# Performance work log

Measured on AMD Instinct MI355X. Metric: run time of the kernel, lower is better.

Reference implementation:

```python
import jax, jax.numpy as jnp
import numpy as np

N_NODES = 10000
N_EDGES = 160000
B = 128
HEADS = 4
DIMS = [36, 128, 256, 512]
NEG_SLOPE = 0.2  # PyG GATConv default


def setup_inputs() -> dict:
    key = jax.random.key(0)
    ks = jax.random.split(key, 32)
    inp = {}
    inp["x"] = jax.random.normal(ks[0], (N_NODES, DIMS[0]), jnp.float32)
    inp["edge_index"] = jax.random.randint(ks[1], (2, N_EDGES), 0, N_NODES)
    inp["batch"] = jnp.sort(jax.random.randint(ks[2], (N_NODES,), 0, B))
    ki = 3
    for i in range(3):
        din, dout = DIMS[i], DIMS[i + 1]
        C = dout // HEADS
        inp[f"gcn_w{i}"] = jax.random.normal(ks[ki], (din, dout), jnp.float32) * (din ** -0.5); ki += 1
        inp[f"gcn_b{i}"] = jnp.zeros((dout,), jnp.float32)
        inp[f"gat_w{i}"] = jax.random.normal(ks[ki], (dout, dout), jnp.float32) * (dout ** -0.5); ki += 1
        inp[f"gat_as{i}"] = jax.random.normal(ks[ki], (HEADS, C), jnp.float32) * 0.1; ki += 1
        inp[f"gat_ad{i}"] = jax.random.normal(ks[ki], (HEADS, C), jnp.float32) * 0.1; ki += 1
        inp[f"gat_b{i}"] = jnp.zeros((dout,), jnp.float32)
    D = DIMS[-1]
    inp["ap_w1"] = jax.random.normal(ks[ki], (D, D // 2), jnp.float32) * (D ** -0.5); ki += 1
    inp["ap_b1"] = jnp.zeros((D // 2,), jnp.float32)
    inp["ap_w2"] = jax.random.normal(ks[ki], (D // 2, 1), jnp.float32) * ((D // 2) ** -0.5); ki += 1
    inp["ap_b2"] = jnp.zeros((1,), jnp.float32)
    return inp


def _gcn(x, w, b, src, dst, n):
    # PyG GCNConv: add self-loops, symmetric deg^-1/2 normalization, bias after agg
    h = x @ w  # [N, dout]
    deg = jax.ops.segment_sum(jnp.ones_like(dst, dtype=h.dtype), dst, n) + 1.0  # incl. self-loop
    dinv = deg ** -0.5
    norm = dinv[src] * dinv[dst]  # [E]
    agg = jax.ops.segment_sum(h[src] * norm[:, None], dst, n)
    agg = agg + h * (dinv * dinv)[:, None]  # self-loop messages
    return agg + b


def _gat(x, w, a_s, a_d, b, src, dst, n):
    # PyG GATConv: self-loops, leaky-relu logits, segment softmax over dst, concat heads
    C = w.shape[1] // HEADS
    h = (x @ w).reshape(n, HEADS, C)
    alpha_src = (h * a_s).sum(-1)  # [N, H]
    alpha_dst = (h * a_d).sum(-1)  # [N, H]
    loop = jnp.arange(n)
    s = jnp.concatenate([src, loop])
    d = jnp.concatenate([dst, loop])
    e = jax.nn.leaky_relu(alpha_src[s] + alpha_dst[d], NEG_SLOPE)  # [E+N, H]
    m = jax.ops.segment_max(e, d, n)
    ex = jnp.exp(e - m[d])
    den = jax.ops.segment_sum(ex, d, n)
    alpha = ex / den[d]  # [E+N, H]
    out = jax.ops.segment_sum(h[s] * alpha[:, :, None], d, n)  # [N, H, C]
    return out.reshape(n, HEADS * C) + b


def _forward(x, edge_index, batch, params, ap_w1, ap_b1, ap_w2, ap_b2):
    src, dst = edge_index[0], edge_index[1]
    n = x.shape[0]
    x_in = x
    n_layers = len(params)
    for i, (gw, gb, aw, a_s, a_d, ab) in enumerate(params):
        h = jax.nn.relu(_gcn(x, gw, gb, src, dst, n))  # dropout is identity in eval
        x = h + _gat(h, aw, a_s, a_d, ab, src, dst, n)
        if i < n_layers - 1:
            if x.shape[-1] == x_in.shape[-1]:
                x = x + x_in
            x_in = x
    # attention pooling (global softmax then per-graph masked renorm)
    a = jnp.tanh(x @ ap_w1 + ap_b1) @ ap_w2 + ap_b2  # [N, 1]
    a = jax.nn.softmax(a, axis=0)
    mask = jax.nn.one_hot(batch, B, dtype=x.dtype)  # [N, B]
    aw_ = a * mask
    aw_ = aw_ / (aw_.sum(0, keepdims=True) + 1e-8)
    graph_emb = aw_.T @ x  # [B, D]
    cnt = jax.ops.segment_sum(jnp.ones((n,), x.dtype), batch, B)
    ssum = jax.ops.segment_sum(x, batch, B)
    mean = ssum / jnp.maximum(cnt, 1.0)[:, None]
    smax = jax.ops.segment_max(x, batch, B)
    return jnp.concatenate([graph_emb, mean, smax, ssum], axis=1)  # [B, 4*D]


def reference(x, edge_index, batch,
              gcn_w0, gcn_b0, gat_w0, gat_as0, gat_ad0, gat_b0,
              gcn_w1, gcn_b1, gat_w1, gat_as1, gat_ad1, gat_b1,
              gcn_w2, gcn_b2, gat_w2, gat_as2, gat_ad2, gat_b2,
              ap_w1, ap_b1, ap_w2, ap_b2):
    params = [
        (gcn_w0, gcn_b0, gat_w0, gat_as0, gat_ad0, gat_b0),
        (gcn_w1, gcn_b1, gat_w1, gat_as1, gat_ad1, gat_b1),
        (gcn_w2, gcn_b2, gat_w2, gat_as2, gat_ad2, gat_b2),
    ]
    return _forward(x, edge_index, batch, params, ap_w1, ap_b1, ap_w2, ap_b2)
```

## Files before the change

### kernel.cpp

```cpp
#include <hip/hip_runtime.h>
#include <math.h>

#define NN 10000
#define NE 160000
#define NB 128
#define NH 4
#define DOUT 512
#define NEG 0.2f
#define CNT_BLKS ((NE + 255) / 256)

typedef __attribute__((ext_vector_type(8))) short short8;
typedef __attribute__((ext_vector_type(4))) float f32x4;
typedef __attribute__((ext_vector_type(4))) unsigned short us4;

__device__ __forceinline__ float leakyf(float v){ return fmaxf(v, NEG*v); }
__device__ __forceinline__ void fma4(float4& a, const float4 v, float w){
  a.x += v.x*w; a.y += v.y*w; a.z += v.z*w; a.w += v.w*w;
}
__device__ __forceinline__ unsigned short f2bf(float f){
  unsigned int u = __float_as_uint(f);
  u += 0x7FFFu + ((u >> 16) & 1u);
  return (unsigned short)(u >> 16);
}
__device__ __forceinline__ float bf2f(unsigned short h){
// ... 7 lines not shown
                                         size_t base, float4 v){
  us4 h, l; unsigned short hh, ll;
  split2(v.x, hh, ll); h[0]=hh; l[0]=ll;
  split2(v.y, hh, ll); h[1]=hh; l[1]=ll;
  split2(v.z, hh, ll); h[2]=hh; l[2]=ll;
  split2(v.w, hh, ll); h[3]=hh; l[3]=ll;
  *(us4*)&H[base] = h;
  *(us4*)&L[base] = l;
}
__device__ __forceinline__ void gl_lds16(const unsigned short* g, unsigned short* l){
  __builtin_amdgcn_global_load_lds(
      (const __attribute__((address_space(1))) unsigned int*)g,
      (__attribute__((address_space(3))) unsigned int*)l, 16, 0, 0);
}

struct AllConv {
  const float* src[7];
  unsigned short* dh[7];
  unsigned short* dl[7];
  int K[7], Mm[7], Kp[7], tot[7];
};

__global__ void k_count_conv(const int* __restrict__ dst, int* __restrict__ cnt,
                             AllConv a, int convTot){
  int bid = blockIdx.x;
  if (bid < CNT_BLKS){
    int e = bid*256 + threadIdx.x;
    if (e < NE) atomicAdd(&cnt[dst[e]], 1);
  } else {
    int idx = (bid - CNT_BLKS)*256 + threadIdx.x;
    if (idx >= convTot) return;
    int j = 0;
    while (idx >= a.tot[j]){ idx -= a.tot[j]; j++; }
    int Kp = a.Kp[j], K = a.K[j], M = a.Mm[j];
    int kk = idx % Kp, m = idx / Kp;
    float v = (kk < K) ? a.src[j][(size_t)kk*M + m] : 0.f;
    unsigned short h, l; split2(v, h, l);
    a.dh[j][idx] = h; a.dl[j][idx] = l;
  }
}

__global__ __launch_bounds__(1024) void k_scan_all(
    const int* __restrict__ cnt, const int* __restrict__ batch,
    int* __restrict__ rowptr, float* __restrict__ dinv,
    int* __restrict__ cursor, float* __restrict__ apre,
    int* __restrict__ starts){
  __shared__ int sh[NN];
  __shared__ int pref[1024];
  int t = threadIdx.x;
  for (int i = t; i < NN; i += 1024) sh[i] = cnt[i];
  if (t <= NB){
    int lo = 0, hi = NN;
    while (lo < hi){ int mid = (lo + hi) >> 1; if (batch[mid] < t) lo = mid + 1; else hi = mid; }
    starts[t] = lo;
  }
  __syncthreads();
  int base = t*10;
  int csum = 0;
#pragma unroll
  for (int k = 0; k < 10; k++){ int i = base + k; if (i < NN) csum += sh[i]; }
  pref[t] = csum; __syncthreads();
  for (int o = 1; o < 1024; o <<= 1){
    int v = (t >= o) ? pref[t - o] : 0;
    __syncthreads();
    pref[t] += v;
    __syncthreads();
  }
  int run = pref[t] - csum;
#pragma unroll
  for (int k = 0; k < 10; k++){
    int i = base + k;
    if (i < NN){
      int c = sh[i];
      rowptr[i] = run;
      run += c;
      dinv[i] = rsqrtf((float)c + 1.f);
      cursor[i] = 0;
      apre[i] = 0.f;
    }
  }
  if (t == 1023) rowptr[NN] = pref[1023];
}

__global__ void k_fill(const int* __restrict__ src, const int* __restrict__ dst,
                       const int* __restrict__ rowptr, int* __restrict__ cursor,
                       int* __restrict__ colidx){
  int e = blockIdx.x*blockDim.x + threadIdx.x;
  if (e >= NE) return;
  int d = dst[e];
  int pos = atomicAdd(&cursor[d], 1);
  colidx[rowptr[d] + pos] = src[e];
}

#define GBM 64
#define GBN 128
#define GBK 64
__global__ __launch_bounds__(256) void k_gemm_bf3(
    const unsigned short* __restrict__ Ah, const unsigned short* __restrict__ Al,
    const unsigned short* __restrict__ Bh, const unsigned short* __restrict__ Bl,
    float* __restrict__ C, int N, int Kp, int M, int mode,
    const float* __restrict__ bias, unsigned short* __restrict__ outH,
    unsigned short* __restrict__ outL,
    const float* __restrict__ a_s, const float* __restrict__ a_d,
    float* __restrict__ as_o, float* __restrict__ ad_o, int Cdim){
  __shared__ unsigned short AsH[2*GBM*32], AsL[2*GBM*32];
  __shared__ unsigned short BsH[2*GBN*32], BsL[2*GBN*32];
  __shared__ float sred[2][GBM][4];
  int gx = M / GBN;
  int gy = (N + GBM - 1) / GBM;
  const int G = 8;
  int bid = blockIdx.x;
  int full = gy / G;
  int bid_full = full * G * gx;
  int by, bx;
  if (bid < bid_full){
    int g = bid / (G*gx); int rem = bid % (G*gx);
    by = g*G + rem % G; bx = rem / G;
  } else {
    int rem = bid - bid_full; int rows = gy - full*G;
    by = full*G + rem % rows; bx = rem / rows;
  }
  int row0 = by * GBM, col0 = bx * GBN;
  int t = threadIdx.x;
  int w = t >> 6, L = t & 63;
  int lm = L & 15, lq = L >> 4;
  int wc = w * 32;
// ... 24 lines not shown
  int nk = Kp / GBK;
  for (int kt = 0; kt < nk; kt++){
    int k0 = kt * GBK;
    if (kt) __syncthreads();
#pragma unroll
    for (int h = 0; h < 2; h++){
      int kh = k0 + h*32;
      gl_lds16(&Ah[(size_t)agrow*Kp + kh + ga*8],  &AsH[h*2048 + w*512]);
      gl_lds16(&Al[(size_t)agrow*Kp + kh + ga*8],  &AsL[h*2048 + w*512]);
      gl_lds16(&Bh[(size_t)bgrow0*Kp + kh + gb0*8], &BsH[h*4096 + w*512]);
      gl_lds16(&Bh[(size_t)bgrow1*Kp + kh + gb1*8], &BsH[h*4096 + (w+4)*512]);
      gl_lds16(&Bl[(size_t)bgrow0*Kp + kh + gb0*8], &BsL[h*4096 + w*512]);
      gl_lds16(&Bl[(size_t)bgrow1*Kp + kh + gb1*8], &BsL[h*4096 + (w+4)*512]);
    }
    __syncthreads();

#pragma unroll
    for (int h = 0; h < 2; h++){
      short8 ah[4], al[4], bh[2], bl[2];
#pragma unroll
      for (int mi = 0; mi < 4; mi++){
        ah[mi] = *(const short8*)&AsH[h*2048 + aoff[mi]];
        al[mi] = *(const short8*)&AsL[h*2048 + aoff[mi]];
      }
#pragma unroll
      for (int ni = 0; ni < 2; ni++){
        bh[ni] = *(const short8*)&BsH[h*4096 + boff[ni]];
        bl[ni] = *(const short8*)&BsL[h*4096 + boff[ni]];
      }
#pragma unroll
      for (int mi = 0; mi < 4; mi++)
// ... 40 lines not shown
    float sA0 = a_s[col0 + wc + lm], sA1 = a_s[col0 + wc + 16 + lm];
    float dA0 = a_d[col0 + wc + lm], dA1 = a_d[col0 + wc + 16 + lm];
#pragma unroll
    for (int mi = 0; mi < 4; mi++)
#pragma unroll
      for (int r = 0; r < 4; r++){
        float vs = acc[mi][0][r]*sA0 + acc[mi][1][r]*sA1;
        float vd = acc[mi][0][r]*dA0 + acc[mi][1][r]*dA1;
#pragma unroll
        for (int o = 1; o <= 8; o <<= 1){
          vs += __shfl_xor(vs, o);
          vd += __shfl_xor(vd, o);
        }
        if (lm == 0){
          int row = mi*16 + lq*4 + r;
          sred[0][row][w] = vs;
          sred[1][row][w] = vd;
        }
      }
    __syncthreads();
    if (t < GBM){
      int n = row0 + t;
      if (n < N){
        int wph = Cdim >> 5;
        int nheads = 4 / wph;
        for (int g = 0; g < nheads; g++){
          float ss = 0.f, dd = 0.f;
          for (int q = 0; q < wph; q++){
            ss += sred[0][t][g*wph + q];
            dd += sred[1][t][g*wph + q];
          }
          int hd = (col0 + g*wph*32) / Cdim;
          as_o[n*NH + hd] = ss;
          ad_o[n*NH + hd] = dd;
        }
      }
    }
  } else if (mode == 3){
    float b0 = bias[col0 + wc + lm], b1v = bias[col0 + wc + 16 + lm];
    float w0v = a_s[col0 + wc + lm], w1v = a_s[col0 + wc + 16 + lm];
#pragma unroll
    for (int mi = 0; mi < 4; mi++)
#pragma unroll
      for (int r = 0; r < 4; r++){
        float v = tanhf(acc[mi][0][r] + b0)*w0v + tanhf(acc[mi][1][r] + b1v)*w1v;
#pragma unroll
        for (int o = 1; o <= 8; o <<= 1) v += __shfl_xor(v, o);
        if (lm == 0) sred[0][mi*16 + lq*4 + r][w] = v;
      }
    __syncthreads();
    if (t < GBM){
      int n = row0 + t;
      if (n < N){
        float s = sred[0][t][0] + sred[0][t][1] + sred[0][t][2] + sred[0][t][3];
        atomicAdd(&as_o[n], s);
      }
    }
  }
}

__global__ __launch_bounds__(256) void k_gcn_pre0(
    const float* __restrict__ x0, const float* __restrict__ dinv,
    const int* __restrict__ rowptr, const int* __restrict__ colidx,
    unsigned short* __restrict__ outH, unsigned short* __restrict__ outL){
  int t = threadIdx.x;
  int sub = t & 15;
  int n = blockIdx.x*16 + (t >> 4);
  if (n >= NN) return;
  int f0 = sub*4;
  bool act = f0 < 36;
  int b = rowptr[n], e = rowptr[n+1];
  float dn = dinv[n];
  float4 a0 = make_float4(0,0,0,0), a1 = make_float4(0,0,0,0);
  float4 a2 = make_float4(0,0,0,0), a3 = make_float4(0,0,0,0);
  if (act){
    float4 sv = *(const float4*)&x0[(size_t)n*36 + f0];
    int j = b;
    for (; j + 7 < e; j += 8){
      int s0 = colidx[j],   s1 = colidx[j+1], s2 = colidx[j+2], s3 = colidx[j+3];
      int s4 = colidx[j+4], s5 = colidx[j+5], s6 = colidx[j+6], s7 = colidx[j+7];
      float w0 = dinv[s0], w1 = dinv[s1], w2 = dinv[s2], w3 = dinv[s3];
      float w4 = dinv[s4], w5 = dinv[s5], w6 = dinv[s6], w7 = dinv[s7];
      float4 v0 = *(const float4*)&x0[(size_t)s0*36 + f0];
      float4 v1 = *(const float4*)&x0[(size_t)s1*36 + f0];
      float4 v2 = *(const float4*)&x0[(size_t)s2*36 + f0];
      float4 v3 = *(const float4*)&x0[(size_t)s3*36 + f0];
      float4 v4 = *(const float4*)&x0[(size_t)s4*36 + f0];
// ... 12 lines not shown
      float4 v1 = *(const float4*)&x0[(size_t)s1*36 + f0];
      float4 v2 = *(const float4*)&x0[(size_t)s2*36 + f0];
      float4 v3 = *(const float4*)&x0[(size_t)s3*36 + f0];
      fma4(a0, v0, w0*dn); fma4(a1, v1, w1*dn);
      fma4(a2, v2, w2*dn); fma4(a3, v3, w3*dn);
    }
    for (; j < e; j++){
      int s = colidx[j];
      float4 v = *(const float4*)&x0[(size_t)s*36 + f0];
      fma4(a0, v, dinv[s]*dn);
    }
    float4 acc = make_float4(a0.x+a1.x+a2.x+a3.x, a0.y+a1.y+a2.y+a3.y,
                             a0.z+a1.z+a2.z+a3.z, a0.w+a1.w+a2.w+a3.w);
    float dn2 = dn*dn;
    acc.x += sv.x*dn2; acc.y += sv.y*dn2; acc.z += sv.z*dn2; acc.w += sv.w*dn2;
    store_hl(outH, outL, (size_t)n*64 + f0, acc);
  } else {
    store_hl(outH, outL, (size_t)n*64 + f0, make_float4(0,0,0,0));
  }
}

__global__ __launch_bounds__(256) void k_gcn_pre(
    const float* __restrict__ xf, const float* __restrict__ dinv,
    const int* __restrict__ rowptr, const int* __restrict__ colidx,
    unsigned short* __restrict__ outH, unsigned short* __restrict__ outL,
    int Kp, int nchunk){
  int bid = blockIdx.x;
  int chunk = bid % nchunk, grp = bid / nchunk;
  int t = threadIdx.x;
  int sub = t & 15;
  int n = grp*16 + (t >> 4);
  if (n >= NN) return;
  int f0 = chunk*64 + sub*4;
  int b = rowptr[n], e = rowptr[n+1];
  float dn = dinv[n];
  float4 sv = *(const float4*)&xf[(size_t)n*Kp + f0];
  float4 a0 = make_float4(0,0,0,0), a1 = make_float4(0,0,0,0);
  float4 a2 = make_float4(0,0,0,0), a3 = make_float4(0,0,0,0);
  int j = b;
  for (; j + 7 < e; j += 8){
    int s0 = colidx[j],   s1 = colidx[j+1], s2 = colidx[j+2], s3 = colidx[j+3];
    int s4 = colidx[j+4], s5 = colidx[j+5], s6 = colidx[j+6], s7 = colidx[j+7];
    float w0 = dinv[s0], w1 = dinv[s1], w2 = dinv[s2], w3 = dinv[s3];
    float w4 = dinv[s4], w5 = dinv[s5], w6 = dinv[s6], w7 = dinv[s7];
    float4 v0 = *(const float4*)&xf[(size_t)s0*Kp + f0];
    float4 v1 = *(const float4*)&xf[(size_t)s1*Kp + f0];
    float4 v2 = *(const float4*)&xf[(size_t)s2*Kp + f0];
    float4 v3 = *(const float4*)&xf[(size_t)s3*Kp + f0];
    float4 v4 = *(const float4*)&xf[(size_t)s4*Kp + f0];
    float4 v5 = *(const float4*)&xf[(size_t)s5*Kp + f0];
// ... 11 lines not shown
    float4 v1 = *(const float4*)&xf[(size_t)s1*Kp + f0];
    float4 v2 = *(const float4*)&xf[(size_t)s2*Kp + f0];
    float4 v3 = *(const float4*)&xf[(size_t)s3*Kp + f0];
    fma4(a0, v0, w0*dn); fma4(a1, v1, w1*dn);
    fma4(a2, v2, w2*dn); fma4(a3, v3, w3*dn);
  }
  for (; j < e; j++){
    int s = colidx[j];
    float4 v = *(const float4*)&xf[(size_t)s*Kp + f0];
    fma4(a0, v, dinv[s]*dn);
  }
  float4 acc = make_float4(a0.x+a1.x+a2.x+a3.x, a0.y+a1.y+a2.y+a3.y,
                           a0.z+a1.z+a2.z+a3.z, a0.w+a1.w+a2.w+a3.w);
  float dn2 = dn*dn;
  acc.x += sv.x*dn2; acc.y += sv.y*dn2; acc.z += sv.z*dn2; acc.w += sv.w*dn2;
  store_hl(outH, outL, (size_t)n*Kp + f0, acc);
}

__global__ __launch_bounds__(256) void k_gat_gather(
    const float* __restrict__ hg, const float* __restrict__ hf,
    const int* __restrict__ rowptr, const int* __restrict__ colidx,
    const float* __restrict__ as_, const float* __restrict__ ad_,
    const float* __restrict__ ab,
    unsigned short* __restrict__ outH, unsigned short* __restrict__ outL,
    float* __restrict__ xf,
    int M, int C, int nchunk){
  int bid = blockIdx.x;
  int chunk = bid % nchunk, grp = bid / nchunk;
  int t = threadIdx.x;
  int sub = t & 15;
  int n = grp*16 + (t >> 4);
  if (n >= NN) return;
  int f0 = chunk*64 + sub*4;
  int hd = f0 / C;
  int b = rowptr[n], e = rowptr[n+1];
  int ai = n*NH + hd;
  float adn = ad_[ai];
  float sl = fminf(fmaxf(leakyf(as_[ai] + adn), -80.f), 80.f);
  float es = __expf(sl);
  float4 sv = *(const float4*)&hg[(size_t)n*M + f0];
  float4 hv = *(const float4*)&hf[(size_t)n*M + f0];
  float4 bb = *(const float4*)&ab[f0];
  float d = es;
  float4 a0 = make_float4(0,0,0,0), a1 = make_float4(0,0,0,0);
  float4 a2 = make_float4(0,0,0,0), a3 = make_float4(0,0,0,0);
  int j = b;
  for (; j + 7 < e; j += 8){
    int s0 = colidx[j],   s1 = colidx[j+1], s2 = colidx[j+2], s3 = colidx[j+3];
    int s4 = colidx[j+4], s5 = colidx[j+5], s6 = colidx[j+6], s7 = colidx[j+7];
    float l0 = leakyf(as_[s0*NH + hd] + adn), l1 = leakyf(as_[s1*NH + hd] + adn);
    float l2 = leakyf(as_[s2*NH + hd] + adn), l3 = leakyf(as_[s3*NH + hd] + adn);
    float l4 = leakyf(as_[s4*NH + hd] + adn), l5 = leakyf(as_[s5*NH + hd] + adn);
    float l6 = leakyf(as_[s6*NH + hd] + adn), l7 = leakyf(as_[s7*NH + hd] + adn);
    float4 v0 = *(const float4*)&hg[(size_t)s0*M + f0];
    float4 v1 = *(const float4*)&hg[(size_t)s1*M + f0];
    float4 v2 = *(const float4*)&hg[(size_t)s2*M + f0];
    float4 v3 = *(const float4*)&hg[(size_t)s3*M + f0];
// ... 15 lines not shown
    int s = colidx[j];
    float l = leakyf(as_[s*NH + hd] + adn);
    float4 v = *(const float4*)&hg[(size_t)s*M + f0];
    float ww = __expf(fminf(fmaxf(l,-80.f),80.f));
    d += ww;
    fma4(a0, v, ww);
  }
  float4 acc = make_float4(a0.x+a1.x+a2.x+a3.x, a0.y+a1.y+a2.y+a3.y,
                           a0.z+a1.z+a2.z+a3.z, a0.w+a1.w+a2.w+a3.w);
  float inv = 1.f/d;
  float4 r = make_float4(
    hv.x + bb.x + (sv.x*es + acc.x)*inv,
    hv.y + bb.y + (sv.y*es + acc.y)*inv,
    hv.z + bb.z + (sv.z*es + acc.z)*inv,
    hv.w + bb.w + (sv.w*es + acc.w)*inv);
  *(float4*)&xf[(size_t)n*M + f0] = r;
  store_hl(outH, outL, (size_t)n*M + f0, r);
}

__global__ __launch_bounds__(512) void k_pool(
    const float* __restrict__ xf,
    const float* __restrict__ apre, const int* __restrict__ starts,
    float* __restrict__ out){
  __shared__ float red[512];
  __shared__ float4 comb[3][4][128];
  int g = blockIdx.x, t = threadIdx.x;
  int b = starts[g], e = starts[g+1];
  float m = -INFINITY;
  for (int n = b + t; n < e; n += 512) m = fmaxf(m, apre[n]);
  red[t] = m; __syncthreads();
  for (int o = 256; o > 0; o >>= 1){
    if (t < o) red[t] = fmaxf(red[t], red[t + o]);
    __syncthreads();
  }
  m = red[0]; __syncthreads();
  float s = 0.f;
  for (int n = b + t; n < e; n += 512) s += __expf(apre[n] - m);
  red[t] = s; __syncthreads();
  for (int o = 256; o > 0; o >>= 1){
    if (t < o) red[t] += red[t + o];
    __syncthreads();
  }
  float inv = 1.f / (red[0] + 1e-8f);
  int lf = t & 127, sl = t >> 7;
  float4 sum = make_float4(0,0,0,0), wacc = make_float4(0,0,0,0);
  float4 mx = make_float4(-INFINITY,-INFINITY,-INFINITY,-INFINITY);
  for (int n = b + sl; n < e; n += 4){
    float4 xv = *(const float4*)&xf[(size_t)n*DOUT + lf*4];
    float p = __expf(apre[n] - m) * inv;
    sum.x += xv.x; sum.y += xv.y; sum.z += xv.z; sum.w += xv.w;
    mx.x = fmaxf(mx.x, xv.x); mx.y = fmaxf(mx.y, xv.y);
    mx.z = fmaxf(mx.z, xv.z); mx.w = fmaxf(mx.w, xv.w);
    fma4(wacc, xv, p);
  }
  comb[0][sl][lf] = wacc; comb[1][sl][lf] = sum; comb[2][sl][lf] = mx;
  __syncthreads();
  if (sl == 0){
#pragma unroll
    for (int q = 1; q < 4; q++){
      float4 w2 = comb[0][q][lf], s2 = comb[1][q][lf], m2 = comb[2][q][lf];
      wacc.x += w2.x; wacc.y += w2.y; wacc.z += w2.z; wacc.w += w2.w;
      sum.x += s2.x; sum.y += s2.y; sum.z += s2.z; sum.w += s2.w;
      mx.x = fmaxf(mx.x, m2.x); mx.y = fmaxf(mx.y, m2.y);
      mx.z = fmaxf(mx.z, m2.z); mx.w = fmaxf(mx.w, m2.w);
    }
    float ic = 1.f / fmaxf((float)(e - b), 1.f);
    float4* o = (float4*)(out + (size_t)g*4*DOUT);
    o[lf]       = wacc;
    o[128 + lf] = make_float4(sum.x*ic, sum.y*ic, sum.z*ic, sum.w*ic);
    o[256 + lf] = mx;
    o[384 + lf] = sum;
  }
}

extern "C" void kernel_launch(void* const* d_in, const int* in_sizes, int n_in,
                              void* d_out, int out_size, void* d_ws, size_t ws_size,
                              hipStream_t stream) {
  const float* x0   = (const float*)d_in[0];
  const int*   ei   = (const int*)d_in[1];
  const int*   src  = ei;
  const int*   dst  = ei + NE;
  const int*   batch= (const int*)d_in[2];
  const float* gw[3]  = {(const float*)d_in[3],  (const float*)d_in[9],  (const float*)d_in[15]};
  const float* gb[3]  = {(const float*)d_in[4],  (const float*)d_in[10], (const float*)d_in[16]};
  const float* aw[3]  = {(const float*)d_in[5],  (const float*)d_in[11], (const float*)d_in[17]};
  const float* asw[3] = {(const float*)d_in[6],  (const float*)d_in[12], (const float*)d_in[18]};
  const float* adw[3] = {(const float*)d_in[7],  (const float*)d_in[13], (const float*)d_in[19]};
  const float* ab[3]  = {(const float*)d_in[8],  (const float*)d_in[14], (const float*)d_in[20]};
  const float* apw1 = (const float*)d_in[21];
  const float* apb1 = (const float*)d_in[22];
  const float* apw2 = (const float*)d_in[23];
  float* out = (float*)d_out;

  char* p = (char*)d_ws;
  auto alloc = [&](size_t bytes) -> void* {
    void* r = (void*)p; p += (bytes + 255) & ~(size_t)255; return r;
  };
  float* f1 = (float*)alloc((size_t)NN*512*4);
  float* hf = (float*)alloc((size_t)NN*512*4);
  float* xf = (float*)alloc((size_t)NN*512*4);
  unsigned short* actH0 = (unsigned short*)alloc((size_t)NN*512*2);
  unsigned short* actL0 = (unsigned short*)alloc((size_t)NN*512*2);
  unsigned short* actH1 = (unsigned short*)alloc((size_t)NN*512*2);
  unsigned short* actL1 = (unsigned short*)alloc((size_t)NN*512*2);
  unsigned short* preH  = (unsigned short*)alloc((size_t)NN*256*2);
  unsigned short* preL  = (unsigned short*)alloc((size_t)NN*256*2);
  const int wK[7]  = {36, 128, 128, 256, 256, 512, 512};
  const int wM[7]  = {128, 128, 256, 256, 512, 512, 256};
  const int wKp[7] = {64, 128, 128, 256, 256, 512, 512};
  const float* wsrc[7] = {gw[0], aw[0], gw[1], aw[1], gw[2], aw[2], apw1};
  unsigned short* wTh[7]; unsigned short* wTl[7];
  for (int i = 0; i < 7; i++){
    size_t sz = (size_t)wM[i]*wKp[i]*2;
    wTh[i] = (unsigned short*)alloc(sz);
    wTl[i] = (unsigned short*)alloc(sz);
  }
  float* dinv = (float*)alloc(NN*4);
  float* as_  = (float*)alloc(NN*NH*4);
  float* ad_  = (float*)alloc(NN*NH*4);
  float* apre = (float*)alloc(NN*4);
  int* rowptr = (int*)alloc((NN+1)*4);
  int* colidx = (int*)alloc((size_t)NE*4);
  int* cnt    = (int*)alloc(NN*4);
  int* cursor = (int*)alloc(NN*4);
  int* starts = (int*)alloc((NB+1)*4);

  AllConv ac;
  int convTot = 0;
  for (int i = 0; i < 7; i++){
    ac.src[i] = wsrc[i]; ac.dh[i] = wTh[i]; ac.dl[i] = wTl[i];
    ac.K[i] = wK[i]; ac.Mm[i] = wM[i]; ac.Kp[i] = wKp[i];
    ac.tot[i] = wKp[i]*wM[i];
    convTot += ac.tot[i];
  }

  hipMemsetAsync(cnt, 0, NN*sizeof(int), stream);
  int convBlks = (convTot + 255) / 256;
  k_count_conv<<<CNT_BLKS + convBlks, 256, 0, stream>>>(dst, cnt, ac, convTot);
  k_scan_all<<<1, 1024, 0, stream>>>(cnt, batch, rowptr, dinv, cursor, apre, starts);
  k_fill<<<(NE+255)/256, 256, 0, stream>>>(src, dst, rowptr, cursor, colidx);

  const int dims[4] = {36, 128, 256, 512};
  const int ngrp = (NN + 15) / 16;
  int wi = 0;
  for (int i = 0; i < 3; i++){
    int Kin = (i == 0) ? 64 : dims[i];
    int M = dims[i+1], C = M/NH;
    int nchunk_in = Kin / 64;
    int nchunk = M / 64;
    int nblk = (M/GBN) * ((NN+GBM-1)/GBM);
    if (i == 0){
      k_gcn_pre0<<<ngrp, 256, 0, stream>>>(x0, dinv, rowptr, colidx, preH, preL);
    } else {
      k_gcn_pre<<<nchunk_in*ngrp, 256, 0, stream>>>(xf, dinv, rowptr, colidx,
                                                    preH, preL, Kin, nchunk_in);
    }
    k_gemm_bf3<<<nblk, 256, 0, stream>>>(preH, preL, wTh[wi], wTl[wi], hf, NN, wKp[wi], M,
                                         1, gb[i], actH0, actL0,
                                         nullptr, nullptr, nullptr, nullptr, C);
    wi++;
    k_gemm_bf3<<<nblk, 256, 0, stream>>>(actH0, actL0, wTh[wi], wTl[wi], f1, NN, wKp[wi], M,
                                         2, nullptr, nullptr, nullptr,
                                         asw[i], adw[i], as_, ad_, C);
    wi++;
    k_gat_gather<<<nchunk*ngrp, 256, 0, stream>>>(f1, hf, rowptr, colidx,
                                                  as_, ad_, ab[i],
                                                  actH1, actL1, xf, M, C, nchunk);
  }

  {
    int nblk = (256/GBN) * ((NN+GBM-1)/GBM);
    k_gemm_bf3<<<nblk, 256, 0, stream>>>(actH1, actL1, wTh[6], wTl[6], nullptr, NN, wKp[6], 256,
                                         3, apb1, nullptr, nullptr,
                                         apw2, nullptr, apre, nullptr, 64);
  }
  k_pool<<<NB, 512, 0, stream>>>(xf, apre, starts, out);
}
```

Baseline: 382.1 us.

## Fuse whole GNN pipeline into one cooperative persistent kernel with degree-sorted node order

Replaces the sequence of about 15 kernel launches with a single cooperative persistent kernel. Stages are separated by grid-wide syncs, and each stage distributes its GEMM, gather and pool tiles over the resident blocks. It adds a degree histogram in the scan that builds a permutation ordering nodes by descending degree, so gather tiles handle nodes of similar degree together and load imbalance drops. It also skips writing bf16 split activations for the first two GAT layers, where they are unused, and splits pooling across two feature halves per graph. The goal is to remove launch gaps and tail effects. The costs are grid-sync overhead, lower occupancy from the larger shared-memory footprint, and a grid capped at 768 blocks. A plain multi-launch fallback is kept in case the cooperative launch fails.

```diff
diff --git a/kernel.cpp b/kernel.cpp
--- a/kernel.cpp
+++ b/kernel.cpp
@@ -1,5 +1,8 @@
 #include <hip/hip_runtime.h>
+#include <hip/hip_cooperative_groups.h>
 #include <math.h>
+
+namespace cg = cooperative_groups;
 
 #define NN 10000
 #define NE 160000
@@ -8,6 +11,24 @@
 #define DOUT 512
 #define NEG 0.2f
 #define CNT_BLKS ((NE + 255) / 256)
+#define GBM 64
+#define GBN 128
+#define GBK 64
+
+#define SM_ASH  0
+#define SM_ASL  8192
+#define SM_BSH  16384
+#define SM_BSL  32768
+#define SM_SRED 49152
+#define SMEM_SZ 51200
+#define SC_SH   0
+#define SC_PREF 40000
+#define SC_HIST 41024
+#define SC_HTMP 43072
+#define SCAN_SZ 45120
+#define PL_RED  0
+#define PL_COMB 1024
+#define POOL_SZ 13312
 
 typedef __attribute__((ext_vector_type(8))) short short8;
 typedef __attribute__((ext_vector_type(4))) float f32x4;
@@ -45,102 +66,110 @@
       (__attribute__((address_space(3))) unsigned int*)l, 16, 0, 0);
 }
 
-struct AllConv {
-  const float* src[7];
-  unsigned short* dh[7];
-  unsigned short* dl[7];
-  int K[7], Mm[7], Kp[7], tot[7];
+struct MegaArgs {
+  const float* x0; const int* src; const int* dst; const int* batch;
+  int* cnt; int* rowptr; int* colidx; int* cursor; int* starts; int* perm;
+  float* dinv; float* apre; float* as_; float* ad_;
+  float* f1; float* hf; float* xf;
+  unsigned short *actH0,*actL0,*actH1,*actL1,*preH,*preL;
+  const unsigned short* wTh[7]; const unsigned short* wTl[7];
+  const float* wsrc[7]; unsigned short* wdh[7]; unsigned short* wdl[7];
+  int wK[7], wM[7], wKp[7], wTot[7]; int convTot;
+  const float* gb[3]; const float* asw[3]; const float* adw[3]; const float* ab[3];
+  const float* apb1; const float* apw2v;
+  float* out;
 };
 
-__global__ void k_count_conv(const int* __restrict__ dst, int* __restrict__ cnt,
-                             AllConv a, int convTot){
-  int bid = blockIdx.x;
-  if (bid < CNT_BLKS){
-    int e = bid*256 + threadIdx.x;
-    if (e < NE) atomicAdd(&cnt[dst[e]], 1);
-  } else {
-    int idx = (bid - CNT_BLKS)*256 + threadIdx.x;
-    if (idx >= convTot) return;
-    int j = 0;
-    while (idx >= a.tot[j]){ idx -= a.tot[j]; j++; }
-    int Kp = a.Kp[j], K = a.K[j], M = a.Mm[j];
-    int kk = idx % Kp, m = idx / Kp;
-    float v = (kk < K) ? a.src[j][(size_t)kk*M + m] : 0.f;
-    unsigned short h, l; split2(v, h, l);
-    a.dh[j][idx] = h; a.dl[j][idx] = l;
-  }
-}
-
-__global__ __launch_bounds__(1024) void k_scan_all(
-    const int* __restrict__ cnt, const int* __restrict__ batch,
-    int* __restrict__ rowptr, float* __restrict__ dinv,
-    int* __restrict__ cursor, float* __restrict__ apre,
-    int* __restrict__ starts){
-  __shared__ int sh[NN];
-  __shared__ int pref[1024];
+__device__ __forceinline__ void dev_conv(const MegaArgs& A, int idx){
+  int j = 0;
+  while (idx >= A.wTot[j]){ idx -= A.wTot[j]; j++; }
+  int Kp = A.wKp[j], K = A.wK[j], M = A.wM[j];
+  int kk = idx % Kp, m = idx / Kp;
+  float v = (kk < K) ? A.wsrc[j][(size_t)kk*M + m] : 0.f;
+  unsigned short h, l; split2(v, h, l);
+  A.wdh[j][idx] = h; A.wdl[j][idx] = l;
+}
+
+__device__ __forceinline__ void dev_fill(const MegaArgs& A, int e){
+  int d = A.dst[e];
+  int pos = atomicAdd(&A.cursor[d], 1);
+  A.colidx[A.rowptr[d] + pos] = A.src[e];
+}
+
+__device__ void dev_scan256(const MegaArgs& A, char* smem){
+  int* sh   = (int*)(smem + SC_SH);
+  int* pref = (int*)(smem + SC_PREF);
+  int* hist = (int*)(smem + SC_HIST);
+  int* htmp = (int*)(smem + SC_HTMP);
   int t = threadIdx.x;
-  for (int i = t; i < NN; i += 1024) sh[i] = cnt[i];
+  for (int i = t; i < NN; i += 256) sh[i] = A.cnt[i];
+  hist[t] = 0; hist[256 + t] = 0;
   if (t <= NB){
     int lo = 0, hi = NN;
-    while (lo < hi){ int mid = (lo + hi) >> 1; if (batch[mid] < t) lo = mid + 1; else hi = mid; }
-    starts[t] = lo;
+    while (lo < hi){ int mid = (lo + hi) >> 1; if (A.batch[mid] < t) lo = mid + 1; else hi = mid; }
+    A.starts[t] = lo;
   }
   __syncthreads();
-  int base = t*10;
-  int csum = 0;
-#pragma unroll
-  for (int k = 0; k < 10; k++){ int i = base + k; if (i < NN) csum += sh[i]; }
+  const int PER = 40;
+  int base = t*PER, csum = 0;
+  for (int k = 0; k < PER; k++){
+    int i = base + k;
+    if (i < NN){ csum += sh[i]; atomicAdd(&hist[511 - min(sh[i], 511)], 1); }
+  }
   pref[t] = csum; __syncthreads();
-  for (int o = 1; o < 1024; o <<= 1){
+  for (int o = 1; o < 256; o <<= 1){
     int v = (t >= o) ? pref[t - o] : 0;
     __syncthreads();
     pref[t] += v;
     __syncthreads();
   }
+  int b0 = hist[2*t], b1 = hist[2*t + 1];
+  int loc = b0 + b1;
+  htmp[t] = loc; __syncthreads();
+  for (int o = 1; o < 256; o <<= 1){
+    int v = (t >= o) ? htmp[t - o] : 0;
+    __syncthreads();
+    htmp[t] += v;
+    __syncthreads();
+  }
+  int ex = htmp[t] - loc;
+  __syncthreads();
+  hist[2*t] = ex; hist[2*t + 1] = ex + b0;
+  __syncthreads();
   int run = pref[t] - csum;
-#pragma unroll
-  for (int k = 0; k < 10; k++){
+  for (int k = 0; k < PER; k++){
     int i = base + k;
     if (i < NN){
       int c = sh[i];
-      rowptr[i] = run;
-      run += c;
-      dinv[i] = rsqrtf((float)c + 1.f);
-      cursor[i] = 0;
-      apre[i] = 0.f;
-    }
-  }
-  if (t == 1023) rowptr[NN] = pref[1023];
-}
-
-__global__ void k_fill(const int* __restrict__ src, const int* __restrict__ dst,
-                       const int* __restrict__ rowptr, int* __restrict__ cursor,
-                       int* __restrict__ colidx){
-  int e = blockIdx.x*blockDim.x + threadIdx.x;
-  if (e >= NE) return;
-  int d = dst[e];
-  int pos = atomicAdd(&cursor[d], 1);
-  colidx[rowptr[d] + pos] = src[e];
-}
-
-#define GBM 64
-#define GBN 128
-#define GBK 64
-__global__ __launch_bounds__(256) void k_gemm_bf3(
+      A.rowptr[i] = run; run += c;
+      A.dinv[i] = rsqrtf((float)c + 1.f);
+      A.cursor[i] = 0;
+      A.apre[i] = 0.f;
+      int pos = atomicAdd(&hist[511 - min(c, 511)], 1);
+      A.perm[pos] = i;
+    }
+  }
+  if (t == 255) A.rowptr[NN] = pref[255];
+}
+
+__device__ void dev_gemm(
     const unsigned short* __restrict__ Ah, const unsigned short* __restrict__ Al,
     const unsigned short* __restrict__ Bh, const unsigned short* __restrict__ Bl,
     float* __restrict__ C, int N, int Kp, int M, int mode,
     const float* __restrict__ bias, unsigned short* __restrict__ outH,
     unsigned short* __restrict__ outL,
     const float* __restrict__ a_s, const float* __restrict__ a_d,
-    float* __restrict__ as_o, float* __restrict__ ad_o, int Cdim){
-  __shared__ unsigned short AsH[2*GBM*32], AsL[2*GBM*32];
-  __shared__ unsigned short BsH[2*GBN*32], BsL[2*GBN*32];
-  __shared__ float sred[2][GBM][4];
+    float* __restrict__ as_o, float* __restrict__ ad_o, int Cdim,
+    char* smem, int bid){
+  unsigned short* AsH = (unsigned short*)(smem + SM_ASH);
+  unsigned short* AsL = (unsigned short*)(smem + SM_ASL);
+  unsigned short* BsH = (unsigned short*)(smem + SM_BSH);
+  unsigned short* BsL = (unsigned short*)(smem + SM_BSL);
+  float* sredf = (float*)(smem + SM_SRED);
+  __syncthreads();
   int gx = M / GBN;
   int gy = (N + GBM - 1) / GBM;
   const int G = 8;
-  int bid = blockIdx.x;
   int full = gy / G;
   int bid_full = full * G * gx;
   int by, bx;
@@ -195,7 +224,6 @@
       gl_lds16(&Bl[(size_t)bgrow1*Kp + kh + gb1*8], &BsL[h*4096 + (w+4)*512]);
     }
     __syncthreads();
-
 #pragma unroll
     for (int h = 0; h < 2; h++){
       short8 ah[4], al[4], bh[2], bl[2];
@@ -266,8 +294,8 @@
         }
         if (lm == 0){
           int row = mi*16 + lq*4 + r;
-          sred[0][row][w] = vs;
-          sred[1][row][w] = vd;
+          sredf[(0*GBM + row)*4 + w] = vs;
+          sredf[(1*GBM + row)*4 + w] = vd;
         }
       }
     __syncthreads();
@@ -279,8 +307,8 @@
         for (int g = 0; g < nheads; g++){
           float ss = 0.f, dd = 0.f;
           for (int q = 0; q < wph; q++){
-            ss += sred[0][t][g*wph + q];
-            dd += sred[1][t][g*wph + q];
+            ss += sredf[(0*GBM + t)*4 + g*wph + q];
+            dd += sredf[(1*GBM + t)*4 + g*wph + q];
           }
           int hd = (col0 + g*wph*32) / Cdim;
           as_o[n*NH + hd] = ss;
@@ -298,31 +326,31 @@
         float v = tanhf(acc[mi][0][r] + b0)*w0v + tanhf(acc[mi][1][r] + b1v)*w1v;
 #pragma unroll
         for (int o = 1; o <= 8; o <<= 1) v += __shfl_xor(v, o);
-        if (lm == 0) sred[0][mi*16 + lq*4 + r][w] = v;
+        if (lm == 0) sredf[(mi*16 + lq*4 + r)*4 + w] = v;
       }
     __syncthreads();
     if (t < GBM){
       int n = row0 + t;
       if (n < N){
-        float s = sred[0][t][0] + sred[0][t][1] + sred[0][t][2] + sred[0][t][3];
+        float s = sredf[t*4+0] + sredf[t*4+1] + sredf[t*4+2] + sredf[t*4+3];
         atomicAdd(&as_o[n], s);
       }
     }
   }
 }
 
-__global__ __launch_bounds__(256) void k_gcn_pre0(
-    const float* __restrict__ x0, const float* __restrict__ dinv,
-    const int* __restrict__ rowptr, const int* __restrict__ colidx,
-    unsigned short* __restrict__ outH, unsigned short* __restrict__ outL){
+__device__ void dev_pre0(const MegaArgs& A, int tile){
   int t = threadIdx.x;
   int sub = t & 15;
-  int n = blockIdx.x*16 + (t >> 4);
-  if (n >= NN) return;
+  int gid = tile*16 + (t >> 4);
+  int n = A.perm[gid];
   int f0 = sub*4;
   bool act = f0 < 36;
-  int b = rowptr[n], e = rowptr[n+1];
-  float dn = dinv[n];
+  int b = A.rowptr[n], e = A.rowptr[n+1];
+  float dn = A.dinv[n];
+  const float* x0 = A.x0;
+  const int* colidx = A.colidx;
+  const float* dinv = A.dinv;
   float4 a0 = make_float4(0,0,0,0), a1 = make_float4(0,0,0,0);
   float4 a2 = make_float4(0,0,0,0), a3 = make_float4(0,0,0,0);
   if (act){
@@ -365,26 +393,24 @@
                              a0.z+a1.z+a2.z+a3.z, a0.w+a1.w+a2.w+a3.w);
     float dn2 = dn*dn;
     acc.x += sv.x*dn2; acc.y += sv.y*dn2; acc.z += sv.z*dn2; acc.w += sv.w*dn2;
-    store_hl(outH, outL, (size_t)n*64 + f0, acc);
+    store_hl(A.preH, A.preL, (size_t)n*64 + f0, acc);
   } else {
-    store_hl(outH, outL, (size_t)n*64 + f0, make_float4(0,0,0,0));
-  }
-}
-
-__global__ __launch_bounds__(256) void k_gcn_pre(
-    const float* __restrict__ xf, const float* __restrict__ dinv,
-    const int* __restrict__ rowptr, const int* __restrict__ colidx,
-    unsigned short* __restrict__ outH, unsigned short* __restrict__ outL,
-    int Kp, int nchunk){
-  int bid = blockIdx.x;
-  int chunk = bid % nchunk, grp = bid / nchunk;
+    store_hl(A.preH, A.preL, (size_t)n*64 + f0, make_float4(0,0,0,0));
+  }
+}
+
+__device__ void dev_pre(const MegaArgs& A, int tile, int Kp, int nchunk){
+  int chunk = tile % nchunk, grp = tile / nchunk;
   int t = threadIdx.x;
   int sub = t & 15;
-  int n = grp*16 + (t >> 4);
-  if (n >= NN) return;
+  int gid = grp*16 + (t >> 4);
+  int n = A.perm[gid];
   int f0 = chunk*64 + sub*4;
-  int b = rowptr[n], e = rowptr[n+1];
-  float dn = dinv[n];
+  int b = A.rowptr[n], e = A.rowptr[n+1];
+  float dn = A.dinv[n];
+  const float* xf = A.xf;
+  const int* colidx = A.colidx;
+  const float* dinv = A.dinv;
   float4 sv = *(const float4*)&xf[(size_t)n*Kp + f0];
   float4 a0 = make_float4(0,0,0,0), a1 = make_float4(0,0,0,0);
   float4 a2 = make_float4(0,0,0,0), a3 = make_float4(0,0,0,0);
@@ -426,33 +452,29 @@
                            a0.z+a1.z+a2.z+a3.z, a0.w+a1.w+a2.w+a3.w);
   float dn2 = dn*dn;
   acc.x += sv.x*dn2; acc.y += sv.y*dn2; acc.z += sv.z*dn2; acc.w += sv.w*dn2;
-  store_hl(outH, outL, (size_t)n*Kp + f0, acc);
-}
-
-__global__ __launch_bounds__(256) void k_gat_gather(
-    const float* __restrict__ hg, const float* __restrict__ hf,
-    const int* __restrict__ rowptr, const int* __restrict__ colidx,
-    const float* __restrict__ as_, const float* __restrict__ ad_,
-    const float* __restrict__ ab,
-    unsigned short* __restrict__ outH, unsigned short* __restrict__ outL,
-    float* __restrict__ xf,
-    int M, int C, int nchunk){
-  int bid = blockIdx.x;
-  int chunk = bid % nchunk, grp = bid / nchunk;
+  store_hl(A.preH, A.preL, (size_t)n*Kp + f0, acc);
+}
+
+__device__ void dev_gat(const MegaArgs& A, int tile, int M, int C, int nchunk, bool writeHL){
+  int chunk = tile % nchunk, grp = tile / nchunk;
   int t = threadIdx.x;
   int sub = t & 15;
-  int n = grp*16 + (t >> 4);
-  if (n >= NN) return;
+  int gid = grp*16 + (t >> 4);
+  int n = A.perm[gid];
   int f0 = chunk*64 + sub*4;
   int hd = f0 / C;
-  int b = rowptr[n], e = rowptr[n+1];
+  int b = A.rowptr[n], e = A.rowptr[n+1];
+  const float* hg = A.f1;
+  const int* colidx = A.colidx;
+  const float* as_ = A.as_;
   int ai = n*NH + hd;
-  float adn = ad_[ai];
+  float adn = A.ad_[ai];
   float sl = fminf(fmaxf(leakyf(as_[ai] + adn), -80.f), 80.f);
   float es = __expf(sl);
   float4 sv = *(const float4*)&hg[(size_t)n*M + f0];
-  float4 hv = *(const float4*)&hf[(size_t)n*M + f0];
-  float4 bb = *(const float4*)&ab[f0];
+  float4 hv = *(const float4*)&A.hf[(size_t)n*M + f0];
+  float4 bb = *(const float4*)&A.ab[0][0];
+  bb = *(const float4*)&A.ab[(M==128)?0:((M==256)?1:2)][f0];
   float d = es;
   float4 a0 = make_float4(0,0,0,0), a1 = make_float4(0,0,0,0);
   float4 a2 = make_float4(0,0,0,0), a3 = make_float4(0,0,0,0);
@@ -498,63 +520,153 @@
     hv.y + bb.y + (sv.y*es + acc.y)*inv,
     hv.z + bb.z + (sv.z*es + acc.z)*inv,
     hv.w + bb.w + (sv.w*es + acc.w)*inv);
-  *(float4*)&xf[(size_t)n*M + f0] = r;
-  store_hl(outH, outL, (size_t)n*M + f0, r);
-}
-
-__global__ __launch_bounds__(512) void k_pool(
-    const float* __restrict__ xf,
-    const float* __restrict__ apre, const int* __restrict__ starts,
-    float* __restrict__ out){
-  __shared__ float red[512];
-  __shared__ float4 comb[3][4][128];
-  int g = blockIdx.x, t = threadIdx.x;
-  int b = starts[g], e = starts[g+1];
+  *(float4*)&A.xf[(size_t)n*M + f0] = r;
+  if (writeHL) store_hl(A.actH1, A.actL1, (size_t)n*M + f0, r);
+}
+
+__device__ void dev_pool(const MegaArgs& A, int tile, char* smem){
+  float* red = (float*)(smem + PL_RED);
+  float4* comb = (float4*)(smem + PL_COMB);
+  int g = tile >> 1, half = tile & 1, t = threadIdx.x;
+  __syncthreads();
+  int b = A.starts[g], e = A.starts[g+1];
+  const float* apre = A.apre;
   float m = -INFINITY;
-  for (int n = b + t; n < e; n += 512) m = fmaxf(m, apre[n]);
+  for (int n = b + t; n < e; n += 256) m = fmaxf(m, apre[n]);
   red[t] = m; __syncthreads();
-  for (int o = 256; o > 0; o >>= 1){
+  for (int o = 128; o > 0; o >>= 1){
     if (t < o) red[t] = fmaxf(red[t], red[t + o]);
     __syncthreads();
   }
   m = red[0]; __syncthreads();
   float s = 0.f;
-  for (int n = b + t; n < e; n += 512) s += __expf(apre[n] - m);
+  for (int n = b + t; n < e; n += 256) s += __expf(apre[n] - m);
   red[t] = s; __syncthreads();
-  for (int o = 256; o > 0; o >>= 1){
+  for (int o = 128; o > 0; o >>= 1){
     if (t < o) red[t] += red[t + o];
     __syncthreads();
   }
   float inv = 1.f / (red[0] + 1e-8f);
-  int lf = t & 127, sl = t >> 7;
+  int lf = t & 63, slc = t >> 6;
+  int fo = half*64 + lf;
   float4 sum = make_float4(0,0,0,0), wacc = make_float4(0,0,0,0);
   float4 mx = make_float4(-INFINITY,-INFINITY,-INFINITY,-INFINITY);
-  for (int n = b + sl; n < e; n += 4){
-    float4 xv = *(const float4*)&xf[(size_t)n*DOUT + lf*4];
+  for (int n = b + slc; n < e; n += 4){
+    float4 xv = *(const float4*)&A.xf[(size_t)n*DOUT + fo*4];
     float p = __expf(apre[n] - m) * inv;
     sum.x += xv.x; sum.y += xv.y; sum.z += xv.z; sum.w += xv.w;
     mx.x = fmaxf(mx.x, xv.x); mx.y = fmaxf(mx.y, xv.y);
     mx.z = fmaxf(mx.z, xv.z); mx.w = fmaxf(mx.w, xv.w);
     fma4(wacc, xv, p);
   }
-  comb[0][sl][lf] = wacc; comb[1][sl][lf] = sum; comb[2][sl][lf] = mx;
+  comb[(0*4 + slc)*64 + lf] = wacc;
+  comb[(1*4 + slc)*64 + lf] = sum;
+  comb[(2*4 + slc)*64 + lf] = mx;
   __syncthreads();
-  if (sl == 0){
+  if (slc == 0){
 #pragma unroll
     for (int q = 1; q < 4; q++){
-      float4 w2 = comb[0][q][lf], s2 = comb[1][q][lf], m2 = comb[2][q][lf];
+      float4 w2 = comb[(0*4+q)*64+lf], s2 = comb[(1*4+q)*64+lf], m2 = comb[(2*4+q)*64+lf];
       wacc.x += w2.x; wacc.y += w2.y; wacc.z += w2.z; wacc.w += w2.w;
       sum.x += s2.x; sum.y += s2.y; sum.z += s2.z; sum.w += s2.w;
       mx.x = fmaxf(mx.x, m2.x); mx.y = fmaxf(mx.y, m2.y);
       mx.z = fmaxf(mx.z, m2.z); mx.w = fmaxf(mx.w, m2.w);
     }
     float ic = 1.f / fmaxf((float)(e - b), 1.f);
-    float4* o = (float4*)(out + (size_t)g*4*DOUT);
-    o[lf]       = wacc;
-    o[128 + lf] = make_float4(sum.x*ic, sum.y*ic, sum.z*ic, sum.w*ic);
-    o[256 + lf] = mx;
-    o[384 + lf] = sum;
-  }
+    float4* o = (float4*)(A.out + (size_t)g*4*DOUT);
+    o[fo]       = wacc;
+    o[128 + fo] = make_float4(sum.x*ic, sum.y*ic, sum.z*ic, sum.w*ic);
+    o[256 + fo] = mx;
+    o[384 + fo] = sum;
+  }
+}
+
+__global__ __launch_bounds__(256) void k_mega(MegaArgs A){
+  cg::grid_group gg = cg::this_grid();
+  __shared__ char smem[SMEM_SZ];
+  int nb = gridDim.x, bid = blockIdx.x, t = threadIdx.x;
+  int stride = nb*256, tid = bid*256 + t;
+
+  for (int i = tid; i < NE; i += stride) atomicAdd(&A.cnt[A.dst[i]], 1);
+  for (int i = tid; i < A.convTot; i += stride) dev_conv(A, i);
+  gg.sync();
+  if (bid == 0) dev_scan256(A, smem);
+  gg.sync();
+  for (int e = tid; e < NE; e += stride) dev_fill(A, e);
+  gg.sync();
+
+  const int dims[4] = {36, 128, 256, 512};
+  for (int layer = 0; layer < 3; layer++){
+    int wi = layer*2;
+    int Kin = (layer == 0) ? 64 : dims[layer];
+    int M = dims[layer+1], C = M/NH;
+    int nin = Kin/64, nch = M/64;
+    int gy = (NN + GBM - 1)/GBM;
+    int nblk = (M/GBN)*gy;
+    if (layer == 0){
+      for (int tl = bid; tl < 625; tl += nb) dev_pre0(A, tl);
+    } else {
+      for (int tl = bid; tl < nin*625; tl += nb) dev_pre(A, tl, Kin, nin);
+    }
+    gg.sync();
+    for (int tl = bid; tl < nblk; tl += nb)
+      dev_gemm(A.preH, A.preL, A.wTh[wi], A.wTl[wi], A.hf, NN, A.wKp[wi], M, 1,
+               A.gb[layer], A.actH0, A.actL0, nullptr, nullptr, nullptr, nullptr, C, smem, tl);
+    gg.sync();
+    for (int tl = bid; tl < nblk; tl += nb)
+      dev_gemm(A.actH0, A.actL0, A.wTh[wi+1], A.wTl[wi+1], A.f1, NN, A.wKp[wi+1], M, 2,
+               nullptr, nullptr, nullptr, A.asw[layer], A.adw[layer], A.as_, A.ad_, C, smem, tl);
+    gg.sync();
+    for (int tl = bid; tl < nch*625; tl += nb) dev_gat(A, tl, M, C, nch, layer == 2);
+    gg.sync();
+  }
+  {
+    int nblk = (256/GBN)*((NN + GBM - 1)/GBM);
+    for (int tl = bid; tl < nblk; tl += nb)
+      dev_gemm(A.actH1, A.actL1, A.wTh[6], A.wTl[6], nullptr, NN, A.wKp[6], 256, 3,
+               A.apb1, nullptr, nullptr, A.apw2v, nullptr, A.apre, nullptr, 64, smem, tl);
+    gg.sync();
+    for (int tl = bid; tl < NB*2; tl += nb) dev_pool(A, tl, smem);
+  }
+}
+
+__global__ void k_count_conv_fb(MegaArgs A){
+  int bid = blockIdx.x;
+  if (bid < CNT_BLKS){
+    int e = bid*256 + threadIdx.x;
+    if (e < NE) atomicAdd(&A.cnt[A.dst[e]], 1);
+  } else {
+    int idx = (bid - CNT_BLKS)*256 + threadIdx.x;
+    if (idx < A.convTot) dev_conv(A, idx);
+  }
+}
+__global__ __launch_bounds__(256) void k_scan_fb(MegaArgs A){
+  __shared__ char s[SCAN_SZ];
+  dev_scan256(A, s);
+}
+__global__ void k_fill_fb(MegaArgs A){
+  int e = blockIdx.x*256 + threadIdx.x;
+  if (e < NE) dev_fill(A, e);
+}
+__global__ __launch_bounds__(256) void k_pre0_fb(MegaArgs A){ dev_pre0(A, blockIdx.x); }
+__global__ __launch_bounds__(256) void k_pre_fb(MegaArgs A, int Kp, int nch){
+  dev_pre(A, blockIdx.x, Kp, nch);
+}
+__global__ __launch_bounds__(256) void k_gemm_fb(
+    const unsigned short* Ah, const unsigned short* Al,
+    const unsigned short* Bh, const unsigned short* Bl,
+    float* C, int N, int Kp, int M, int mode, const float* bias,
+    unsigned short* outH, unsigned short* outL,
+    const float* a_s, const float* a_d, float* as_o, float* ad_o, int Cdim){
+  __shared__ char s[SMEM_SZ];
+  dev_gemm(Ah, Al, Bh, Bl, C, N, Kp, M, mode, bias, outH, outL, a_s, a_d, as_o, ad_o, Cdim, s, blockIdx.x);
+}
+__global__ __launch_bounds__(256) void k_gat_fb(MegaArgs A, int M, int C, int nch, int wHL){
+  dev_gat(A, blockIdx.x, M, C, nch, wHL != 0);
+}
+__global__ __launch_bounds__(256) void k_pool_fb(MegaArgs A){
+  __shared__ char s[POOL_SZ];
+  dev_pool(A, blockIdx.x, s);
 }
 
 extern "C" void kernel_launch(void* const* d_in, const int* in_sizes, int n_in,
@@ -580,83 +692,89 @@
   auto alloc = [&](size_t bytes) -> void* {
     void* r = (void*)p; p += (bytes + 255) & ~(size_t)255; return r;
   };
-  float* f1 = (float*)alloc((size_t)NN*512*4);
-  float* hf = (float*)alloc((size_t)NN*512*4);
-  float* xf = (float*)alloc((size_t)NN*512*4);
-  unsigned short* actH0 = (unsigned short*)alloc((size_t)NN*512*2);
-  unsigned short* actL0 = (unsigned short*)alloc((size_t)NN*512*2);
-  unsigned short* actH1 = (unsigned short*)alloc((size_t)NN*512*2);
-  unsigned short* actL1 = (unsigned short*)alloc((size_t)NN*512*2);
-  unsigned short* preH  = (unsigned short*)alloc((size_t)NN*256*2);
-  unsigned short* preL  = (unsigned short*)alloc((size_t)NN*256*2);
+  MegaArgs A;
+  A.x0 = x0; A.src = src; A.dst = dst; A.batch = batch; A.out = out;
+  A.f1 = (float*)alloc((size_t)NN*512*4);
+  A.hf = (float*)alloc((size_t)NN*512*4);
+  A.xf = (float*)alloc((size_t)NN*512*4);
+  A.actH0 = (unsigned short*)alloc((size_t)NN*512*2);
+  A.actL0 = (unsigned short*)alloc((size_t)NN*512*2);
+  A.actH1 = (unsigned short*)alloc((size_t)NN*512*2);
+  A.actL1 = (unsigned short*)alloc((size_t)NN*512*2);
+  A.preH  = (unsigned short*)alloc((size_t)NN*256*2);
+  A.preL  = (unsigned short*)alloc((size_t)NN*256*2);
   const int wK[7]  = {36, 128, 128, 256, 256, 512, 512};
   const int wM[7]  = {128, 128, 256, 256, 512, 512, 256};
   const int wKp[7] = {64, 128, 128, 256, 256, 512, 512};
   const float* wsrc[7] = {gw[0], aw[0], gw[1], aw[1], gw[2], aw[2], apw1};
-  unsigned short* wTh[7]; unsigned short* wTl[7];
+  int convTot = 0;
   for (int i = 0; i < 7; i++){
     size_t sz = (size_t)wM[i]*wKp[i]*2;
-    wTh[i] = (unsigned short*)alloc(sz);
-    wTl[i] = (unsigned short*)alloc(sz);
-  }
-  float* dinv = (float*)alloc(NN*4);
-  float* as_  = (float*)alloc(NN*NH*4);
-  float* ad_  = (float*)alloc(NN*NH*4);
-  float* apre = (float*)alloc(NN*4);
-  int* rowptr = (int*)alloc((NN+1)*4);
-  int* colidx = (int*)alloc((size_t)NE*4);
-  int* cnt    = (int*)alloc(NN*4);
-  int* cursor = (int*)alloc(NN*4);
-  int* starts = (int*)alloc((NB+1)*4);
-
-  AllConv ac;
-  int convTot = 0;
-  for (int i = 0; i < 7; i++){
-    ac.src[i] = wsrc[i]; ac.dh[i] = wTh[i]; ac.dl[i] = wTl[i];
-    ac.K[i] = wK[i]; ac.Mm[i] = wM[i]; ac.Kp[i] = wKp[i];
-    ac.tot[i] = wKp[i]*wM[i];
-    convTot += ac.tot[i];
-  }
-
-  hipMemsetAsync(cnt, 0, NN*sizeof(int), stream);
+    unsigned short* th = (unsigned short*)alloc(sz);
+    unsigned short* tl = (unsigned short*)alloc(sz);
+    A.wTh[i] = th; A.wTl[i] = tl; A.wdh[i] = th; A.wdl[i] = tl;
+    A.wsrc[i] = wsrc[i];
+    A.wK[i] = wK[i]; A.wM[i] = wM[i]; A.wKp[i] = wKp[i];
+    A.wTot[i] = wKp[i]*wM[i];
+    convTot += A.wTot[i];
+  }
+  A.convTot = convTot;
+  A.dinv = (float*)alloc(NN*4);
+  A.as_  = (float*)alloc(NN*NH*4);
+  A.ad_  = (float*)alloc(NN*NH*4);
+  A.apre = (float*)alloc(NN*4);
+  A.rowptr = (int*)alloc((NN+1)*4);
+  A.colidx = (int*)alloc((size_t)NE*4);
+  A.cnt    = (int*)alloc(NN*4);
+  A.cursor = (int*)alloc(NN*4);
+  A.starts = (int*)alloc((NB+1)*4);
+  A.perm   = (int*)alloc(NN*4);
+  for (int i = 0; i < 3; i++){
+    A.gb[i] = gb[i]; A.asw[i] = asw[i]; A.adw[i] = adw[i]; A.ab[i] = ab[i];
+  }
+  A.apb1 = apb1; A.apw2v = apw2;
+
+  hipMemsetAsync(A.cnt, 0, NN*sizeof(int), stream);
+
+  int perCU = 0;
+  hipError_t qe = hipOccupancyMaxActiveBlocksPerMultiprocessor(&perCU, k_mega, 256, 0);
+  if (qe != hipSuccess || perCU < 1) perCU = 1;
+  int grid = perCU * 256;
+  if (grid > 768) grid = 768;
+  void* kargs[] = { (void*)&A };
+  hipError_t ce = hipLaunchCooperativeKernel((void*)k_mega, dim3(grid), dim3(256),
+                                             kargs, 0, stream);
+  if (ce == hipSuccess) return;
+
   int convBlks = (convTot + 255) / 256;
-  k_count_conv<<<CNT_BLKS + convBlks, 256, 0, stream>>>(dst, cnt, ac, convTot);
-  k_scan_all<<<1, 1024, 0, stream>>>(cnt, batch, rowptr, dinv, cursor, apre, starts);
-  k_fill<<<(NE+255)/256, 256, 0, stream>>>(src, dst, rowptr, cursor, colidx);
-
+  k_count_conv_fb<<<CNT_BLKS + convBlks, 256, 0, stream>>>(A);
+  k_scan_fb<<<1, 256, 0, stream>>>(A);
+  k_fill_fb<<<(NE+255)/256, 256, 0, stream>>>(A);
   const int dims[4] = {36, 128, 256, 512};
-  const int ngrp = (NN + 15) / 16;
-  int wi = 0;
   for (int i = 0; i < 3; i++){
+    int wi = i*2;
     int Kin = (i == 0) ? 64 : dims[i];
     int M = dims[i+1], C = M/NH;
-    int nchunk_in = Kin / 64;
-    int nchunk = M / 64;
+    int nin = Kin/64, nch = M/64;
     int nblk = (M/GBN) * ((NN+GBM-1)/GBM);
     if (i == 0){
-      k_gcn_pre0<<<ngrp, 256, 0, stream>>>(x0, dinv, rowptr, colidx, preH, preL);
+      k_pre0_fb<<<625, 256, 0, stream>>>(A);
     } else {
-      k_gcn_pre<<<nchunk_in*ngrp, 256, 0, stream>>>(xf, dinv, rowptr, colidx,
-                                                    preH, preL, Kin, nchunk_in);
-    }
-    k_gemm_bf3<<<nblk, 256, 0, stream>>>(preH, preL, wTh[wi], wTl[wi], hf, NN, wKp[wi], M,
-                                         1, gb[i], actH0, actL0,
-                                         nullptr, nullptr, nullptr, nullptr, C);
-    wi++;
-    k_gemm_bf3<<<nblk, 256, 0, stream>>>(actH0, actL0, wTh[wi], wTl[wi], f1, NN, wKp[wi], M,
-                                         2, nullptr, nullptr, nullptr,
-                                         asw[i], adw[i], as_, ad_, C);
-    wi++;
-    k_gat_gather<<<nchunk*ngrp, 256, 0, stream>>>(f1, hf, rowptr, colidx,
-                                                  as_, ad_, ab[i],
-                                                  actH1, actL1, xf, M, C, nchunk);
-  }
-
+      k_pre_fb<<<nin*625, 256, 0, stream>>>(A, Kin, nin);
+    }
+    k_gemm_fb<<<nblk, 256, 0, stream>>>(A.preH, A.preL, A.wTh[wi], A.wTl[wi], A.hf,
+                                        NN, A.wKp[wi], M, 1, A.gb[i], A.actH0, A.actL0,
+                                        nullptr, nullptr, nullptr, nullptr, C);
+    k_gemm_fb<<<nblk, 256, 0, stream>>>(A.actH0, A.actL0, A.wTh[wi+1], A.wTl[wi+1], A.f1,
+                                        NN, A.wKp[wi+1], M, 2, nullptr, nullptr, nullptr,
+                                        A.asw[i], A.adw[i], A.as_, A.ad_, C);
+    k_gat_fb<<<nch*625, 256, 0, stream>>>(A, M, C, nch, (i == 2) ? 1 : 0);
+  }
   {
     int nblk = (256/GBN) * ((NN+GBM-1)/GBM);
-    k_gemm_bf3<<<nblk, 256, 0, stream>>>(actH1, actL1, wTh[6], wTl[6], nullptr, NN, wKp[6], 256,
-                                         3, apb1, nullptr, nullptr,
-                                         apw2, nullptr, apre, nullptr, 64);
-  }
-  k_pool<<<NB, 512, 0, stream>>>(xf, apre, starts, out);
-}
+    k_gemm_fb<<<nblk, 256, 0, stream>>>(A.actH1, A.actL1, A.wTh[6], A.wTl[6], nullptr,
+                                        NN, A.wKp[6], 256, 3, A.apb1, nullptr, nullptr,
+                                        A.apw2v, nullptr, A.apre, nullptr, 64);
+  }
+  k_pool_fb<<<NB*2, 256, 0, stream>>>(A);
+}
```

New measurement: 1.066 ms. 179% more time.
